# Kernel optimization log

Measured on AMD Instinct MI355X. Metric: run time of the kernel, lower is better.

Reference implementation:

```python
import jax, jax.numpy as jnp
import numpy as np

B, S, D, H = 2, 2048, 1024, 16
DK = D // H

def setup_inputs() -> dict:
    key = jax.random.key(0)
    ks = jax.random.split(key, 12)
    s = 1.0 / np.sqrt(D)
    return {
        "q": jax.random.normal(ks[0], (B, S, D), jnp.float32),
        "k": jax.random.normal(ks[1], (B, S, D), jnp.float32),
        "v": jax.random.normal(ks[2], (B, S, D), jnp.float32),
        "mask": jnp.ones((1, 1, S, S), jnp.int32),
        "Wq": jax.random.normal(ks[3], (D, D), jnp.float32) * s,
        "bq": jnp.zeros((D,), jnp.float32),
        "Wk": jax.random.normal(ks[4], (D, D), jnp.float32) * s,
        "bk": jnp.zeros((D,), jnp.float32),
        "Wv": jax.random.normal(ks[5], (D, D), jnp.float32) * s,
        "bv": jnp.zeros((D,), jnp.float32),
        "Wo": jax.random.normal(ks[6], (D, D), jnp.float32) * s,
        "bo": jnp.zeros((D,), jnp.float32),
    }

def reference(q, k, v, mask, Wq, bq, Wk, bk, Wv, bv, Wo, bo):
    # projections (torch Linear: x @ W^T + b)
    Q = q @ Wq.T + bq
    K = k @ Wk.T + bk
    V = v @ Wv.T + bv
    # split heads: [B,S,D] -> [B,H,S,DK]
    def split(x):
        return x.reshape(B, S, H, DK).transpose(0, 2, 1, 3)
    Qh, Kh, Vh = split(Q), split(K), split(V)
    scores = jnp.einsum('bhqd,bhkd->bhqk', Qh, Kh) / jnp.sqrt(jnp.float32(DK))
    scores = jnp.where(mask == 0, jnp.float32(-1e9), scores)
    attn = jax.nn.softmax(scores, axis=-1)  # dropout p=0.0 -> identity
    x = jnp.einsum('bhqk,bhkd->bhqd', attn, Vh)
    x = x.transpose(0, 2, 1, 3).reshape(B, S, D)
    return x @ Wo.T + bo
```

## Files before the change

kernel.cpp:

```cpp
#include <hip/hip_runtime.h>
#include <hip/hip_bf16.h>
#include <stdint.h>

#define B_    2
#define S_    2048
#define D_    1024
#define H_    16
#define NTOK  (B_ * S_)

typedef __attribute__((ext_vector_type(8))) short bf16x8;
typedef __attribute__((ext_vector_type(4))) float f32x4;
typedef __attribute__((ext_vector_type(2))) float float2v;
typedef __attribute__((ext_vector_type(2))) __bf16 bfv2;

static __device__ __forceinline__ unsigned int pkbf(float a, float b) {
    float2v fv = {a, b};
    bfv2 r = __builtin_convertvector(fv, bfv2);
    unsigned int u;
    __builtin_memcpy(&u, &r, 4);
    return u;
}

using g_cu32 = __attribute__((address_space(1))) const unsigned int;
using l_u32  = __attribute__((address_space(3))) unsigned int;
static __device__ __forceinline__ void gld16(const void* g, void* l) {
    __builtin_amdgcn_global_load_lds((g_cu32*)g, (l_u32*)l, 16, 0, 0);
}

template<int N> static __device__ __forceinline__ void wait_vm() {
    if constexpr (N == 0)      asm volatile("s_waitcnt vmcnt(0)" ::: "memory");
    else if constexpr (N == 2) asm volatile("s_waitcnt vmcnt(2)" ::: "memory");
    else if constexpr (N == 3) asm volatile("s_waitcnt vmcnt(3)" ::: "memory");
    else if constexpr (N == 4) asm volatile("s_waitcnt vmcnt(4)" ::: "memory");
}

#define QN ((size_t)NTOK * D_)
#define WN ((size_t)D_ * D_)

__global__ __launch_bounds__(256) void prep_kernel(
    const float* __restrict__ q, const float* __restrict__ k, const float* __restrict__ v,
    const float* __restrict__ Wq, const float* __restrict__ Wk,
    const float* __restrict__ Wv, const float* __restrict__ Wo,
    const int* __restrict__ mask,
    unsigned short* __restrict__ qb, unsigned short* __restrict__ kb,
    unsigned short* __restrict__ vb, unsigned short* __restrict__ wqb,
    unsigned short* __restrict__ wkb, unsigned short* __restrict__ wvb,
    unsigned short* __restrict__ wob, int* __restrict__ flags) {
    __shared__ int anyz;
    if (blockIdx.x < 8192) {
        size_t i = ((size_t)blockIdx.x * 256 + threadIdx.x) * 8;
        const float* s; unsigned short* d; size_t off;
        if (i < QN)          { s = q; d = qb; off = i; }
        else if (i < 2 * QN) { s = k; d = kb; off = i - QN; }
        else if (i < 3 * QN) { s = v; d = vb; off = i - 2 * QN; }
        else {
            size_t j = i - 3 * QN;
            int wi = (int)(j >> 20);
            s = (wi == 0) ? Wq : (wi == 1) ? Wk : (wi == 2) ? Wv : Wo;
            d = (wi == 0) ? wqb : (wi == 1) ? wkb : (wi == 2) ? wvb : wob;
            off = j & (WN - 1);
        }
        float4 a = *(const float4*)(s + off);
        float4 b = *(const float4*)(s + off + 4);
        uint4 pk;
        pk.x = pkbf(a.x, a.y); pk.y = pkbf(a.z, a.w);
        pk.z = pkbf(b.x, b.y); pk.w = pkbf(b.z, b.w);
        *(uint4*)(d + off) = pk;
    } else {
        if (threadIdx.x == 0) anyz = 0;
        __syncthreads();
        int bid2 = blockIdx.x - 8192;
        const int qt = bid2 >> 5, kt = bid2 & 31;
        int az = 0;
        for (int i = threadIdx.x; i < 64 * 64; i += 256) {
            int r = i >> 6, c = i & 63;
            az |= (mask[(size_t)(qt * 64 + r) * S_ + kt * 64 + c] == 0) ? 1 : 0;
        }
        if (az) atomicOr(&anyz, 1);
        __syncthreads();
        if (threadIdx.x == 0) flags[qt * 32 + kt] = anyz;
    }
}

struct GemmArgs {
    const unsigned short* A[3];
    const unsigned short* W[3];
    const float* bias[3];
    void* C[3];
    int mode[3];
    float scale[3];
};

__global__ __launch_bounds__(512, 2) void gemm_bigM(GemmArgs ga) {
    constexpr int NK = D_ / 32;
    constexpr int AG = 16;
    constexpr int NG = 24;

    const int bid = blockIdx.x;
    const int l = (bid & 7) * 48 + (bid >> 3);
    const int z = l >> 7;
    const int r = l & 127;
    const int bx = r & 15;
    const int by = r >> 4;

    const unsigned short* __restrict__ A = ga.A[z];
    const unsigned short* __restrict__ W = ga.W[z];
    const float* __restrict__ bias = ga.bias[z];
    void* C = ga.C[z];
    const int mode = ga.mode[z];
    const float scl = ga.scale[z];

    __shared__ unsigned short Ls[3][NG * 512];

    const int t    = threadIdx.x;
    const int lane = t & 63;
    const int w    = t >> 6;
    const int fr   = lane & 15;
    const int kq   = lane >> 4;
    const int wrow = w >> 1;
    const int wcol = w & 1;
    const int m0 = bx * 256, n0 = by * 128;

    const int sc = lane >> 4;
    const int sr = lane & 15;

    const unsigned short* gA0 = A + (size_t)(m0 + (2 * w) * 16 + sr) * D_ + sc * 8;
    const unsigned short* gA1 = gA0 + 16 * D_;
    const unsigned short* gB0 = W + (size_t)(n0 + w * 16 + sr) * D_ + sc * 8;
    const int lA0 = (2 * w) * 512, lA1 = (2 * w + 1) * 512, lB0 = (AG + w) * 512;

    int aOff[4], bOff[4];
#pragma unroll
    for (int mi = 0; mi < 4; ++mi) aOff[mi] = (wrow * 4 + mi) * 512 + (kq * 16 + fr) * 8;
#pragma unroll
    for (int ni = 0; ni < 4; ++ni) bOff[ni] = (AG + wcol * 4 + ni) * 512 + (kq * 16 + fr) * 8;

    f32x4 acc[4][4];
#pragma unroll
    for (int i = 0; i < 4; ++i)
#pragma unroll
        for (int j = 0; j < 4; ++j) acc[i][j] = (f32x4)0.0f;

    auto stage = [&](int buf) {
        gld16(gA0, &Ls[buf][lA0]);
        gld16(gA1, &Ls[buf][lA1]);
        gld16(gB0, &Ls[buf][lB0]);
        gA0 += 32; gA1 += 32; gB0 += 32;
    };

    const bool swp = (mode != 2);

    stage(0);
    stage(1);
    int cur = 0;
    for (int k0 = 0; k0 < NK; ++k0) {
        __builtin_amdgcn_sched_barrier(0);
        if (k0 < NK - 1) wait_vm<3>();
        else             wait_vm<0>();
        __builtin_amdgcn_s_barrier();
        __builtin_amdgcn_sched_barrier(0);
        if (k0 + 2 < NK) {
            int pf = (cur >= 1) ? cur - 1 : cur + 2;
            stage(pf);
        }

        bf16x8 af[4], bfr[4];
#pragma unroll
        for (int mi = 0; mi < 4; ++mi) af[mi] = *(const bf16x8*)&Ls[cur][aOff[mi]];
#pragma unroll
        for (int ni = 0; ni < 4; ++ni) bfr[ni] = *(const bf16x8*)&Ls[cur][bOff[ni]];
        if (swp) {
#pragma unroll
            for (int mi = 0; mi < 4; ++mi)
#pragma unroll
                for (int ni = 0; ni < 4; ++ni)
                    acc[mi][ni] = __builtin_amdgcn_mfma_f32_16x16x32_bf16(
                        bfr[ni], af[mi], acc[mi][ni], 0, 0, 0);
        } else {
#pragma unroll
            for (int mi = 0; mi < 4; ++mi)
#pragma unroll
                for (int ni = 0; ni < 4; ++ni)
                    acc[mi][ni] = __builtin_amdgcn_mfma_f32_16x16x32_bf16(
                        af[mi], bfr[ni], acc[mi][ni], 0, 0, 0);
        }
        cur = (cur < 2) ? cur + 1 : 0;
    }

    if (mode == 2) {
        unsigned short* Co = (unsigned short*)C;
#pragma unroll
        for (int ni = 0; ni < 4; ++ni) {
            int col = n0 + wcol * 64 + ni * 16 + fr;
            float bv = bias[col];
            int hh = col >> 6, d = col & 63;
#pragma unroll
            for (int mi = 0; mi < 4; ++mi) {
                int tok = m0 + wrow * 64 + mi * 16 + kq * 4;
                int bb = tok >> 11, sbase = tok & (S_ - 1);
                uint2 pk;
                pk.x = pkbf((acc[mi][ni][0] + bv) * scl, (acc[mi][ni][1] + bv) * scl);
                pk.y = pkbf((acc[mi][ni][2] + bv) * scl, (acc[mi][ni][3] + bv) * scl);
                *(uint2*)(Co + ((size_t)((bb * H_ + hh) * 64 + d)) * S_ + sbase) = pk;
            }
        }
    } else {
        unsigned short* Co = (unsigned short*)C;
#pragma unroll
        for (int ni = 0; ni < 4; ++ni) {
            int nb = n0 + wcol * 64 + ni * 16 + kq * 4;
            float4 b4 = *(const float4*)&bias[nb];
#pragma unroll
            for (int mi = 0; mi < 4; ++mi) {
                int m = m0 + wrow * 64 + mi * 16 + fr;
                uint2 pk;
                pk.x = pkbf((acc[mi][ni][0] + b4.x) * scl, (acc[mi][ni][1] + b4.y) * scl);
                pk.y = pkbf((acc[mi][ni][2] + b4.z) * scl, (acc[mi][ni][3] + b4.w) * scl);
                *(uint2*)(Co + (size_t)m * D_ + nb) = pk;
            }
        }
    }
}

__global__ __launch_bounds__(256, 3) void gemm_out(GemmArgs ga) {
    constexpr int NK = D_ / 32;
    const int bid = blockIdx.x;
    const int l = (bid & 7) * 32 + (bid >> 3);
    const int bx = l & 31;
    const int by = l >> 5;

    const unsigned short* __restrict__ A = ga.A[0];
    const unsigned short* __restrict__ W = ga.W[0];
    const float* __restrict__ bias = ga.bias[0];
    float* Co = (float*)ga.C[0];

    __shared__ unsigned short As[3][8 * 512];
    __shared__ unsigned short Bs[3][8 * 512];

    const int t    = threadIdx.x;
    const int lane = t & 63;
    const int w    = t >> 6;
    const int fr   = lane & 15;
    const int kq   = lane >> 4;
    const int wrow = w >> 1, wcol = w & 1;
    const int m0 = bx * 128, n0 = by * 128;

    const int sc = lane >> 4;
    const int sr = lane & 15;

    const unsigned short* ga0 = A + (size_t)(m0 + (2 * w) * 16 + sr) * D_ + sc * 8;
    const unsigned short* ga1 = ga0 + 16 * D_;
    const unsigned short* gw0 = W + (size_t)(n0 + (2 * w) * 16 + sr) * D_ + sc * 8;
    const unsigned short* gw1 = gw0 + 16 * D_;
    const int la0 = (2 * w) * 512, la1 = (2 * w + 1) * 512;
    const int lw0 = (2 * w) * 512, lw1 = (2 * w + 1) * 512;

    int aOff[4], bOff[4];
#pragma unroll
    for (int mi = 0; mi < 4; ++mi) aOff[mi] = (wrow * 4 + mi) * 512 + (kq * 16 + fr) * 8;
#pragma unroll
    for (int ni = 0; ni < 4; ++ni) bOff[ni] = (wcol * 4 + ni) * 512 + (kq * 16 + fr) * 8;

    f32x4 acc[4][4];
#pragma unroll
    for (int i = 0; i < 4; ++i)
#pragma unroll
        for (int j = 0; j < 4; ++j) acc[i][j] = (f32x4)0.0f;

    auto stage = [&](int buf) {
        gld16(ga0, &As[buf][la0]);
        gld16(ga1, &As[buf][la1]);
        gld16(gw0, &Bs[buf][lw0]);
        gld16(gw1, &Bs[buf][lw1]);
        ga0 += 32; ga1 += 32; gw0 += 32; gw1 += 32;
    };

    stage(0);
    stage(1);
    int cur = 0;
    for (int k0 = 0; k0 < NK; ++k0) {
        __builtin_amdgcn_sched_barrier(0);
        if (k0 < NK - 1) wait_vm<4>();
        else             wait_vm<0>();
        __builtin_amdgcn_s_barrier();
        __builtin_amdgcn_sched_barrier(0);
        if (k0 + 2 < NK) {
            int pf = (cur >= 1) ? cur - 1 : cur + 2;
            stage(pf);
        }

        bf16x8 af[4], bfr[4];
#pragma unroll
        for (int mi = 0; mi < 4; ++mi) af[mi] = *(const bf16x8*)&As[cur][aOff[mi]];
#pragma unroll
        for (int ni = 0; ni < 4; ++ni) bfr[ni] = *(const bf16x8*)&Bs[cur][bOff[ni]];
#pragma unroll
        for (int mi = 0; mi < 4; ++mi)
#pragma unroll
            for (int ni = 0; ni < 4; ++ni)
                acc[mi][ni] = __builtin_amdgcn_mfma_f32_16x16x32_bf16(
                    bfr[ni], af[mi], acc[mi][ni], 0, 0, 0);
        cur = (cur < 2) ? cur + 1 : 0;
    }

#pragma unroll
    for (int ni = 0; ni < 4; ++ni) {
        int nb = n0 + wcol * 64 + ni * 16 + kq * 4;
        float4 b4 = *(const float4*)&bias[nb];
#pragma unroll
        for (int mi = 0; mi < 4; ++mi) {
            int m = m0 + wrow * 64 + mi * 16 + fr;
            float4 o4;
            o4.x = acc[mi][ni][0] + b4.x;
            o4.y = acc[mi][ni][1] + b4.y;
            o4.z = acc[mi][ni][2] + b4.z;
            o4.w = acc[mi][ni][3] + b4.w;
            *(float4*)(Co + (size_t)m * D_ + nb) = o4;
        }
    }
}

__global__ __launch_bounds__(512, 2) void flash4(
    const unsigned short* __restrict__ Qb, const unsigned short* __restrict__ Kb,
    const unsigned short* __restrict__ Vtg, const int* __restrict__ mask,
    const int* __restrict__ flags, unsigned short* __restrict__ Xb) {
    __shared__ unsigned short Ks[3][4096];
    __shared__ unsigned short Vs[3][4096];
    __shared__ unsigned short Ps[16384];

    const int t    = threadIdx.x;
    const int lane = t & 63;
    const int w    = t >> 6;
    const int fr   = lane & 15;
    const int kq   = lane >> 4;
    const int bid = blockIdx.x;
    const int swb = ((bid & 7) << 5) | (bid >> 3);
    const int qt = swb & 7, hd = (swb >> 3) & 15, b = swb >> 7;
    const int q0 = qt * 256;
    const int swz = fr & 7;

    bf16x8 qf[2][2];
#pragma unroll
    for (int qc = 0; qc < 2; ++qc) {
        const unsigned short* qrow_p =
            Qb + (size_t)(b * S_ + q0 + w * 32 + qc * 16 + fr) * D_ + hd * 64;
        qf[qc][0] = *(const bf16x8*)(qrow_p + kq * 8);
        qf[qc][1] = *(const bf16x8*)(qrow_p + 32 + kq * 8);
    }

    unsigned int fmask[2];
#pragma unroll
    for (int qc = 0; qc < 2; ++qc) {
        int qt64 = qt * 4 + ((2 * w + qc) >> 2);
        int fl = (lane < 32) ? flags[qt64 * 32 + lane] : 0;
        fmask[qc] = (unsigned int)__ballot(fl != 0);
    }

    const unsigned short* kptr =
        Kb + (size_t)(b * S_ + (w >> 1) * 16 + fr) * D_ + hd * 64 + (w & 1) * 32 + kq * 8;
    const unsigned short* vptr =
        Vtg + ((size_t)((b * H_ + hd) * 64 + (w >> 1) * 16 + fr)) * S_ + (w & 1) * 32 + kq * 8;

    gld16(kptr, (char*)&Ks[0][0] + w * 1024);
    gld16(vptr, (char*)&Vs[0][0] + w * 1024);
    gld16(kptr + (size_t)64 * D_, (char*)&Ks[1][0] + w * 1024);
    gld16(vptr + 64,              (char*)&Vs[1][0] + w * 1024);
    const unsigned short* kpf = kptr + (size_t)128 * D_;
    const unsigned short* vpf = vptr + 128;

    unsigned short* pswr[2][4];
    const unsigned short* psrd[2][2];
#pragma unroll
    for (int qc = 0; qc < 2; ++qc) {
        int row = w * 32 + qc * 16 + fr;
#pragma unroll
        for (int mi = 0; mi < 4; ++mi) {
            int chunk = mi * 2 + (kq >> 1);
            pswr[qc][mi] = &Ps[row * 64 + ((chunk ^ swz) << 3) + ((kq & 1) << 2)];
        }
#pragma unroll
        for (int kk = 0; kk < 2; ++kk) {
            int c = kk * 4 + kq;
            psrd[qc][kk] = &Ps[row * 64 + ((c ^ swz) << 3)];
        }
    }

    const f32x4 zf = (f32x4)0.0f;
    f32x4 o[2][4];
#pragma unroll
    for (int qc = 0; qc < 2; ++qc)
#pragma unroll
        for (int i = 0; i < 4; ++i) o[qc][i] = zf;
    float2v l2[2];
    l2[0] = (float2v){0.0f, 0.0f};
    l2[1] = (float2v){0.0f, 0.0f};

    auto attn_step = [&](int cur, int kt) {
        f32x4 st[2][4];
#pragma unroll
        for (int mi = 0; mi < 4; ++mi) {
            bf16x8 a = *(const bf16x8*)&Ks[cur][mi * 1024 + (kq * 16 + fr) * 8];
            st[0][mi] = __builtin_amdgcn_mfma_f32_16x16x32_bf16(a, qf[0][0], zf, 0, 0, 0);
            st[1][mi] = __builtin_amdgcn_mfma_f32_16x16x32_bf16(a, qf[1][0], zf, 0, 0, 0);
        }
#pragma unroll
        for (int mi = 0; mi < 4; ++mi) {
            bf16x8 a = *(const bf16x8*)&Ks[cur][mi * 1024 + ((4 + kq) * 16 + fr) * 8];
            st[0][mi] = __builtin_amdgcn_mfma_f32_16x16x32_bf16(a, qf[0][1], st[0][mi], 0, 0, 0);
            st[1][mi] = __builtin_amdgcn_mfma_f32_16x16x32_bf16(a, qf[1][1], st[1][mi], 0, 0, 0);
        }

#pragma unroll
        for (int qc = 0; qc < 2; ++qc) {
            if ((fmask[qc] >> kt) & 1u) {
#pragma unroll
                for (int mi = 0; mi < 4; ++mi) {
                    int4 mv = *(const int4*)&mask[(size_t)(q0 + w * 32 + qc * 16 + fr) * S_ +
                                                  kt * 64 + mi * 16 + kq * 4];
                    if (mv.x == 0) st[qc][mi][0] = -3e8f;
                    if (mv.y == 0) st[qc][mi][1] = -3e8f;
                    if (mv.z == 0) st[qc][mi][2] = -3e8f;
                    if (mv.w == 0) st[qc][mi][3] = -3e8f;
                }
            }
        }

#pragma unroll
        for (int qc = 0; qc < 2; ++qc)
#pragma unroll
            for (int mi = 0; mi < 4; ++mi) {
                float e0 = __builtin_amdgcn_exp2f(st[qc][mi][0]);
                float e1 = __builtin_amdgcn_exp2f(st[qc][mi][1]);
                float e2 = __builtin_amdgcn_exp2f(st[qc][mi][2]);
                float e3 = __builtin_amdgcn_exp2f(st[qc][mi][3]);
                l2[qc] += (float2v){e0, e1} + (float2v){e2, e3};
                uint2 pk;
                pk.x = pkbf(e0, e1);
                pk.y = pkbf(e2, e3);
                *(uint2*)pswr[qc][mi] = pk;
            }

#pragma unroll
        for (int kk = 0; kk < 2; ++kk) {
            bf16x8 pb0 = *(const bf16x8*)psrd[0][kk];
            bf16x8 pb1 = *(const bf16x8*)psrd[1][kk];
#pragma unroll
            for (int mi = 0; mi < 4; ++mi) {
                bf16x8 a = *(const bf16x8*)&Vs[cur][mi * 1024 + ((kk * 4 + kq) * 16 + fr) * 8];
                o[0][mi] = __builtin_amdgcn_mfma_f32_16x16x32_bf16(a, pb0, o[0][mi], 0, 0, 0);
                o[1][mi] = __builtin_amdgcn_mfma_f32_16x16x32_bf16(a, pb1, o[1][mi], 0, 0, 0);
            }
        }
    };

    int cur = 0;
    for (int kt = 0; kt < 31; ++kt) {
        __builtin_amdgcn_sched_barrier(0);
        wait_vm<2>();
        __builtin_amdgcn_s_barrier();
        __builtin_amdgcn_sched_barrier(0);
        if (kt < 30) {
            int pf = (cur >= 1) ? cur - 1 : cur + 2;
            gld16(kpf, (char*)&Ks[pf][0] + w * 1024);
            gld16(vpf, (char*)&Vs[pf][0] + w * 1024);
            kpf += (size_t)64 * D_;
            vpf += 64;
        }
        attn_step(cur, kt);
        cur = (cur < 2) ? cur + 1 : 0;
    }
    __builtin_amdgcn_sched_barrier(0);
    wait_vm<0>();
    __builtin_amdgcn_s_barrier();
    __builtin_amdgcn_sched_barrier(0);
    attn_step(cur, 31);

#pragma unroll
    for (int qc = 0; qc < 2; ++qc) {
        float l_i = l2[qc].x + l2[qc].y;
        l_i += __shfl_xor(l_i, 16, 64);
        l_i += __shfl_xor(l_i, 32, 64);
        float rl = 1.0f / l_i;
#pragma unroll
        for (int mi = 0; mi < 4; ++mi) {
            uint2 pk;
            pk.x = pkbf(o[qc][mi][0] * rl, o[qc][mi][1] * rl);
            pk.y = pkbf(o[qc][mi][2] * rl, o[qc][mi][3] * rl);
            *(uint2*)(Xb + (size_t)(b * S_ + q0 + w * 32 + qc * 16 + fr) * D_ +
                      hd * 64 + mi * 16 + kq * 4) = pk;
        }
    }
}

extern "C" void kernel_launch(void* const* d_in, const int* in_sizes, int n_in,
                              void* d_out, int out_size, void* d_ws, size_t ws_size,
                              hipStream_t stream) {
    const float* q    = (const float*)d_in[0];
    const float* k    = (const float*)d_in[1];
    const float* v    = (const float*)d_in[2];
    const int*   mask = (const int*)d_in[3];
    const float* Wq   = (const float*)d_in[4];
    const float* bq   = (const float*)d_in[5];
    const float* Wk   = (const float*)d_in[6];
    const float* bk   = (const float*)d_in[7];
    const float* Wv   = (const float*)d_in[8];
    const float* bv   = (const float*)d_in[9];
    const float* Wo   = (const float*)d_in[10];
    const float* bo   = (const float*)d_in[11];
    float* out = (float*)d_out;

    unsigned short* qb  = (unsigned short*)d_ws;
    unsigned short* kb  = qb + QN;
    unsigned short* vb  = kb + QN;
    unsigned short* Qf  = vb + QN;
    unsigned short* Kf  = Qf + QN;
    unsigned short* Vt  = Kf + QN;
    unsigned short* wqb = Vt + QN;
    unsigned short* wkb = wqb + WN;
    unsigned short* wvb = wkb + WN;
    unsigned short* wob = wvb + WN;
    int* flags = (int*)(wob + WN);

    const float SC = 0.18033688011112042f;

    prep_kernel<<<9216, 256, 0, stream>>>(q, k, v, Wq, Wk, Wv, Wo, mask,
                                          qb, kb, vb, wqb, wkb, wvb, wob, flags);

    GemmArgs g1;
    g1.A[0] = qb;  g1.W[0] = wqb; g1.bias[0] = bq; g1.C[0] = Qf; g1.mode[0] = 1; g1.scale[0] = SC;
    g1.A[1] = kb;  g1.W[1] = wkb; g1.bias[1] = bk; g1.C[1] = Kf; g1.mode[1] = 1; g1.scale[1] = 1.0f;
    g1.A[2] = vb;  g1.W[2] = wvb; g1.bias[2] = bv; g1.C[2] = Vt; g1.mode[2] = 2; g1.scale[2] = 1.0f;
    gemm_bigM<<<384, 512, 0, stream>>>(g1);

    flash4<<<256, 512, 0, stream>>>(Qf, Kf, Vt, mask, flags, Qf);

    GemmArgs g2;
    g2.A[0] = Qf; g2.W[0] = wob; g2.bias[0] = bo; g2.C[0] = out; g2.mode[0] = 0; g2.scale[0] = 1.0f;
    g2.A[1] = g2.A[2] = nullptr; g2.W[1] = g2.W[2] = nullptr;
    g2.bias[1] = g2.bias[2] = nullptr; g2.C[1] = g2.C[2] = nullptr;
    g2.mode[1] = g2.mode[2] = 0; g2.scale[1] = g2.scale[2] = 1.0f;
    gemm_out<<<256, 256, 0, stream>>>(g2);
}
```

Baseline: 272.8 us.

## Enlarge QKV GEMM tile to 256x256 with BK=64 double buffering

```diff
diff --git a/kernel.cpp b/kernel.cpp
--- a/kernel.cpp
+++ b/kernel.cpp
@@ -30,8 +30,11 @@
 template<int N> static __device__ __forceinline__ void wait_vm() {
     if constexpr (N == 0)      asm volatile("s_waitcnt vmcnt(0)" ::: "memory");
     else if constexpr (N == 2) asm volatile("s_waitcnt vmcnt(2)" ::: "memory");
-    else if constexpr (N == 3) asm volatile("s_waitcnt vmcnt(3)" ::: "memory");
     else if constexpr (N == 4) asm volatile("s_waitcnt vmcnt(4)" ::: "memory");
+    else if constexpr (N == 8) asm volatile("s_waitcnt vmcnt(8)" ::: "memory");
+}
+static __device__ __forceinline__ void wait_lgkm0() {
+    asm volatile("s_waitcnt lgkmcnt(0)" ::: "memory");
 }
 
 #define QN ((size_t)NTOK * D_)
@@ -91,17 +94,15 @@
     float scale[3];
 };
 
-__global__ __launch_bounds__(512, 2) void gemm_bigM(GemmArgs ga) {
-    constexpr int NK = D_ / 32;
-    constexpr int AG = 16;
-    constexpr int NG = 24;
+__global__ __launch_bounds__(512, 2) void gemm_qkv(GemmArgs ga) {
+    constexpr int NK = D_ / 64;
 
     const int bid = blockIdx.x;
-    const int l = (bid & 7) * 48 + (bid >> 3);
-    const int z = l >> 7;
-    const int r = l & 127;
-    const int bx = r & 15;
-    const int by = r >> 4;
+    const int l = (bid & 7) * 24 + (bid >> 3);
+    const int z = l >> 6;
+    const int r = l & 63;
+    const int bx = r >> 2;
+    const int by = r & 3;
 
     const unsigned short* __restrict__ A = ga.A[z];
     const unsigned short* __restrict__ W = ga.W[z];
@@ -110,81 +111,118 @@
     const int mode = ga.mode[z];
     const float scl = ga.scale[z];
 
-    __shared__ unsigned short Ls[3][NG * 512];
+    __shared__ unsigned short As[2][16384];
+    __shared__ unsigned short Bs[2][16384];
 
     const int t    = threadIdx.x;
     const int lane = t & 63;
     const int w    = t >> 6;
     const int fr   = lane & 15;
     const int kq   = lane >> 4;
-    const int wrow = w >> 1;
-    const int wcol = w & 1;
-    const int m0 = bx * 256, n0 = by * 128;
+    const int wrow = w >> 2;
+    const int wcol = w & 3;
+    const int m0 = bx * 256, n0 = by * 256;
 
     const int sc = lane >> 4;
     const int sr = lane & 15;
 
-    const unsigned short* gA0 = A + (size_t)(m0 + (2 * w) * 16 + sr) * D_ + sc * 8;
-    const unsigned short* gA1 = gA0 + 16 * D_;
-    const unsigned short* gB0 = W + (size_t)(n0 + w * 16 + sr) * D_ + sc * 8;
-    const int lA0 = (2 * w) * 512, lA1 = (2 * w + 1) * 512, lB0 = (AG + w) * 512;
-
-    int aOff[4], bOff[4];
-#pragma unroll
-    for (int mi = 0; mi < 4; ++mi) aOff[mi] = (wrow * 4 + mi) * 512 + (kq * 16 + fr) * 8;
-#pragma unroll
-    for (int ni = 0; ni < 4; ++ni) bOff[ni] = (AG + wcol * 4 + ni) * 512 + (kq * 16 + fr) * 8;
-
-    f32x4 acc[4][4];
-#pragma unroll
-    for (int i = 0; i < 4; ++i)
+    const unsigned short* gA[4];
+    const unsigned short* gB[4];
+    int loA[4], loB[4];
+#pragma unroll
+    for (int j = 0; j < 4; ++j) {
+        int g = w * 4 + j;
+        int kh = g >> 4, rb = g & 15;
+        gA[j] = A + (size_t)(m0 + rb * 16 + sr) * D_ + kh * 32 + sc * 8;
+        gB[j] = W + (size_t)(n0 + rb * 16 + sr) * D_ + kh * 32 + sc * 8;
+        loA[j] = g * 512;
+        loB[j] = g * 512;
+    }
+
+    int aOff[2][8], bOff[2][4];
+#pragma unroll
+    for (int kk = 0; kk < 2; ++kk) {
+#pragma unroll
+        for (int mi = 0; mi < 8; ++mi)
+            aOff[kk][mi] = (kk * 16 + wrow * 8 + mi) * 512 + (kq * 16 + fr) * 8;
+#pragma unroll
+        for (int ni = 0; ni < 4; ++ni)
+            bOff[kk][ni] = (kk * 16 + wcol * 4 + ni) * 512 + (kq * 16 + fr) * 8;
+    }
+
+    f32x4 acc[8][4];
+#pragma unroll
+    for (int i = 0; i < 8; ++i)
 #pragma unroll
         for (int j = 0; j < 4; ++j) acc[i][j] = (f32x4)0.0f;
 
     auto stage = [&](int buf) {
-        gld16(gA0, &Ls[buf][lA0]);
-        gld16(gA1, &Ls[buf][lA1]);
-        gld16(gB0, &Ls[buf][lB0]);
-        gA0 += 32; gA1 += 32; gB0 += 32;
+#pragma unroll
+        for (int j = 0; j < 4; ++j) {
+            gld16(gA[j], &As[buf][loA[j]]);
+            gld16(gB[j], &Bs[buf][loB[j]]);
+            gA[j] += 64; gB[j] += 64;
+        }
     };
 
     const bool swp = (mode != 2);
 
     stage(0);
     stage(1);
-    int cur = 0;
     for (int k0 = 0; k0 < NK; ++k0) {
-        __builtin_amdgcn_sched_barrier(0);
-        if (k0 < NK - 1) wait_vm<3>();
+        const int cur = k0 & 1;
+        __builtin_amdgcn_sched_barrier(0);
+        if (k0 < NK - 1) wait_vm<8>();
         else             wait_vm<0>();
         __builtin_amdgcn_s_barrier();
         __builtin_amdgcn_sched_barrier(0);
-        if (k0 + 2 < NK) {
-            int pf = (cur >= 1) ? cur - 1 : cur + 2;
-            stage(pf);
-        }
-
-        bf16x8 af[4], bfr[4];
-#pragma unroll
-        for (int mi = 0; mi < 4; ++mi) af[mi] = *(const bf16x8*)&Ls[cur][aOff[mi]];
-#pragma unroll
-        for (int ni = 0; ni < 4; ++ni) bfr[ni] = *(const bf16x8*)&Ls[cur][bOff[ni]];
-        if (swp) {
-#pragma unroll
-            for (int mi = 0; mi < 4; ++mi)
+
+        {
+            bf16x8 bfr[4];
+#pragma unroll
+            for (int ni = 0; ni < 4; ++ni) bfr[ni] = *(const bf16x8*)&Bs[cur][bOff[0][ni]];
+#pragma unroll
+            for (int mi = 0; mi < 8; ++mi) {
+                bf16x8 a = *(const bf16x8*)&As[cur][aOff[0][mi]];
+                if (swp) {
+#pragma unroll
+                    for (int ni = 0; ni < 4; ++ni)
+                        acc[mi][ni] = __builtin_amdgcn_mfma_f32_16x16x32_bf16(
+                            bfr[ni], a, acc[mi][ni], 0, 0, 0);
+                } else {
+#pragma unroll
+                    for (int ni = 0; ni < 4; ++ni)
+                        acc[mi][ni] = __builtin_amdgcn_mfma_f32_16x16x32_bf16(
+                            a, bfr[ni], acc[mi][ni], 0, 0, 0);
+                }
+            }
+        }
+
+        bf16x8 af1[8], bf1[4];
+#pragma unroll
+        for (int ni = 0; ni < 4; ++ni) bf1[ni] = *(const bf16x8*)&Bs[cur][bOff[1][ni]];
+#pragma unroll
+        for (int mi = 0; mi < 8; ++mi) af1[mi] = *(const bf16x8*)&As[cur][aOff[1][mi]];
+
+        wait_lgkm0();
+        __builtin_amdgcn_sched_barrier(0);
+        __builtin_amdgcn_s_barrier();
+        if (k0 + 2 < NK) stage(cur);
+
+#pragma unroll
+        for (int mi = 0; mi < 8; ++mi) {
+            if (swp) {
 #pragma unroll
                 for (int ni = 0; ni < 4; ++ni)
                     acc[mi][ni] = __builtin_amdgcn_mfma_f32_16x16x32_bf16(
-                        bfr[ni], af[mi], acc[mi][ni], 0, 0, 0);
-        } else {
-#pragma unroll
-            for (int mi = 0; mi < 4; ++mi)
+                        bf1[ni], af1[mi], acc[mi][ni], 0, 0, 0);
+            } else {
 #pragma unroll
                 for (int ni = 0; ni < 4; ++ni)
                     acc[mi][ni] = __builtin_amdgcn_mfma_f32_16x16x32_bf16(
-                        af[mi], bfr[ni], acc[mi][ni], 0, 0, 0);
-        }
-        cur = (cur < 2) ? cur + 1 : 0;
+                        af1[mi], bf1[ni], acc[mi][ni], 0, 0, 0);
+            }
+        }
     }
 
     if (mode == 2) {
@@ -195,8 +233,8 @@
             float bv = bias[col];
             int hh = col >> 6, d = col & 63;
 #pragma unroll
-            for (int mi = 0; mi < 4; ++mi) {
-                int tok = m0 + wrow * 64 + mi * 16 + kq * 4;
+            for (int mi = 0; mi < 8; ++mi) {
+                int tok = m0 + wrow * 128 + mi * 16 + kq * 4;
                 int bb = tok >> 11, sbase = tok & (S_ - 1);
                 uint2 pk;
                 pk.x = pkbf((acc[mi][ni][0] + bv) * scl, (acc[mi][ni][1] + bv) * scl);
@@ -211,8 +249,8 @@
             int nb = n0 + wcol * 64 + ni * 16 + kq * 4;
             float4 b4 = *(const float4*)&bias[nb];
 #pragma unroll
-            for (int mi = 0; mi < 4; ++mi) {
-                int m = m0 + wrow * 64 + mi * 16 + fr;
+            for (int mi = 0; mi < 8; ++mi) {
+                int m = m0 + wrow * 128 + mi * 16 + fr;
                 uint2 pk;
                 pk.x = pkbf((acc[mi][ni][0] + b4.x) * scl, (acc[mi][ni][1] + b4.y) * scl);
                 pk.y = pkbf((acc[mi][ni][2] + b4.z) * scl, (acc[mi][ni][3] + b4.w) * scl);
@@ -530,7 +568,7 @@
     g1.A[0] = qb;  g1.W[0] = wqb; g1.bias[0] = bq; g1.C[0] = Qf; g1.mode[0] = 1; g1.scale[0] = SC;
     g1.A[1] = kb;  g1.W[1] = wkb; g1.bias[1] = bk; g1.C[1] = Kf; g1.mode[1] = 1; g1.scale[1] = 1.0f;
     g1.A[2] = vb;  g1.W[2] = wvb; g1.bias[2] = bv; g1.C[2] = Vt; g1.mode[2] = 2; g1.scale[2] = 1.0f;
-    gemm_bigM<<<384, 512, 0, stream>>>(g1);
+    gemm_qkv<<<192, 512, 0, stream>>>(g1);
 
     flash4<<<256, 512, 0, stream>>>(Qf, Kf, Vt, mask, flags, Qf);
 
```

Measured after the change: 310.9 us. +14.0%, slower.

## Shrink projection GEMM and flash attention tiles to 256-thread blocks

Applied to the files above, without the earlier changes.

```diff
diff --git a/kernel.cpp b/kernel.cpp
--- a/kernel.cpp
+++ b/kernel.cpp
@@ -29,13 +29,14 @@
 
 template<int N> static __device__ __forceinline__ void wait_vm() {
     if constexpr (N == 0)      asm volatile("s_waitcnt vmcnt(0)" ::: "memory");
-    else if constexpr (N == 2) asm volatile("s_waitcnt vmcnt(2)" ::: "memory");
-    else if constexpr (N == 3) asm volatile("s_waitcnt vmcnt(3)" ::: "memory");
     else if constexpr (N == 4) asm volatile("s_waitcnt vmcnt(4)" ::: "memory");
 }
 
 #define QN ((size_t)NTOK * D_)
 #define WN ((size_t)D_ * D_)
+
+struct SwapT { static constexpr bool value = true; };
+struct NoSwapT { static constexpr bool value = false; };
 
 __global__ __launch_bounds__(256) void prep_kernel(
     const float* __restrict__ q, const float* __restrict__ k, const float* __restrict__ v,
@@ -91,18 +92,9 @@
     float scale[3];
 };
 
-__global__ __launch_bounds__(512, 2) void gemm_bigM(GemmArgs ga) {
+__global__ __launch_bounds__(256, 3) void gemm_async(GemmArgs ga) {
     constexpr int NK = D_ / 32;
-    constexpr int AG = 16;
-    constexpr int NG = 24;
-
-    const int bid = blockIdx.x;
-    const int l = (bid & 7) * 48 + (bid >> 3);
-    const int z = l >> 7;
-    const int r = l & 127;
-    const int bx = r & 15;
-    const int by = r >> 4;
-
+    const int z = blockIdx.z;
     const unsigned short* __restrict__ A = ga.A[z];
     const unsigned short* __restrict__ W = ga.W[z];
     const float* __restrict__ bias = ga.bias[z];
@@ -110,30 +102,32 @@
     const int mode = ga.mode[z];
     const float scl = ga.scale[z];
 
-    __shared__ unsigned short Ls[3][NG * 512];
+    __shared__ unsigned short As[3][8 * 512];
+    __shared__ unsigned short Bs[3][8 * 512];
 
     const int t    = threadIdx.x;
     const int lane = t & 63;
     const int w    = t >> 6;
     const int fr   = lane & 15;
     const int kq   = lane >> 4;
-    const int wrow = w >> 1;
-    const int wcol = w & 1;
-    const int m0 = bx * 256, n0 = by * 128;
+    const int wrow = w >> 1, wcol = w & 1;
+    const int m0 = blockIdx.x * 128, n0 = blockIdx.y * 128;
 
     const int sc = lane >> 4;
     const int sr = lane & 15;
 
-    const unsigned short* gA0 = A + (size_t)(m0 + (2 * w) * 16 + sr) * D_ + sc * 8;
-    const unsigned short* gA1 = gA0 + 16 * D_;
-    const unsigned short* gB0 = W + (size_t)(n0 + w * 16 + sr) * D_ + sc * 8;
-    const int lA0 = (2 * w) * 512, lA1 = (2 * w + 1) * 512, lB0 = (AG + w) * 512;
+    const unsigned short* ga0 = A + (size_t)(m0 + (2 * w) * 16 + sr) * D_ + sc * 8;
+    const unsigned short* ga1 = ga0 + 16 * D_;
+    const unsigned short* gw0 = W + (size_t)(n0 + (2 * w) * 16 + sr) * D_ + sc * 8;
+    const unsigned short* gw1 = gw0 + 16 * D_;
+    const int la0 = (2 * w) * 512, la1 = (2 * w + 1) * 512;
+    const int lw0 = (2 * w) * 512, lw1 = (2 * w + 1) * 512;
 
     int aOff[4], bOff[4];
 #pragma unroll
     for (int mi = 0; mi < 4; ++mi) aOff[mi] = (wrow * 4 + mi) * 512 + (kq * 16 + fr) * 8;
 #pragma unroll
-    for (int ni = 0; ni < 4; ++ni) bOff[ni] = (AG + wcol * 4 + ni) * 512 + (kq * 16 + fr) * 8;
+    for (int ni = 0; ni < 4; ++ni) bOff[ni] = (wcol * 4 + ni) * 512 + (kq * 16 + fr) * 8;
 
     f32x4 acc[4][4];
 #pragma unroll
@@ -142,50 +136,56 @@
         for (int j = 0; j < 4; ++j) acc[i][j] = (f32x4)0.0f;
 
     auto stage = [&](int buf) {
-        gld16(gA0, &Ls[buf][lA0]);
-        gld16(gA1, &Ls[buf][lA1]);
-        gld16(gB0, &Ls[buf][lB0]);
-        gA0 += 32; gA1 += 32; gB0 += 32;
+        gld16(ga0, &As[buf][la0]);
+        gld16(ga1, &As[buf][la1]);
+        gld16(gw0, &Bs[buf][lw0]);
+        gld16(gw1, &Bs[buf][lw1]);
+        ga0 += 32; ga1 += 32; gw0 += 32; gw1 += 32;
     };
 
-    const bool swp = (mode != 2);
-
-    stage(0);
-    stage(1);
-    int cur = 0;
-    for (int k0 = 0; k0 < NK; ++k0) {
+    auto kloop = [&](auto swc) {
+        constexpr bool SW = decltype(swc)::value;
+        auto mma_step = [&](int cur) {
+            bf16x8 af[4], bfr[4];
+#pragma unroll
+            for (int mi = 0; mi < 4; ++mi) af[mi] = *(const bf16x8*)&As[cur][aOff[mi]];
+#pragma unroll
+            for (int ni = 0; ni < 4; ++ni) bfr[ni] = *(const bf16x8*)&Bs[cur][bOff[ni]];
+#pragma unroll
+            for (int mi = 0; mi < 4; ++mi)
+#pragma unroll
+                for (int ni = 0; ni < 4; ++ni) {
+                    if constexpr (SW)
+                        acc[mi][ni] = __builtin_amdgcn_mfma_f32_16x16x32_bf16(
+                            bfr[ni], af[mi], acc[mi][ni], 0, 0, 0);
+                    else
+                        acc[mi][ni] = __builtin_amdgcn_mfma_f32_16x16x32_bf16(
+                            af[mi], bfr[ni], acc[mi][ni], 0, 0, 0);
+                }
+        };
+
+        stage(0);
+        stage(1);
+        int cur = 0;
+        for (int k0 = 0; k0 < NK - 1; ++k0) {
+            __builtin_amdgcn_sched_barrier(0);
+            wait_vm<4>();
+            __builtin_amdgcn_s_barrier();
+            __builtin_amdgcn_sched_barrier(0);
+            if (k0 + 2 < NK) {
+                int pf = (cur >= 1) ? cur - 1 : cur + 2;
+                stage(pf);
+            }
+            mma_step(cur);
+            cur = (cur < 2) ? cur + 1 : 0;
+        }
         __builtin_amdgcn_sched_barrier(0);
-        if (k0 < NK - 1) wait_vm<3>();
-        else             wait_vm<0>();
+        wait_vm<0>();
         __builtin_amdgcn_s_barrier();
         __builtin_amdgcn_sched_barrier(0);
-        if (k0 + 2 < NK) {
-            int pf = (cur >= 1) ? cur - 1 : cur + 2;
-            stage(pf);
-        }
-
-        bf16x8 af[4], bfr[4];
-#pragma unroll
-        for (int mi = 0; mi < 4; ++mi) af[mi] = *(const bf16x8*)&Ls[cur][aOff[mi]];
-#pragma unroll
-        for (int ni = 0; ni < 4; ++ni) bfr[ni] = *(const bf16x8*)&Ls[cur][bOff[ni]];
-        if (swp) {
-#pragma unroll
-            for (int mi = 0; mi < 4; ++mi)
-#pragma unroll
-                for (int ni = 0; ni < 4; ++ni)
-                    acc[mi][ni] = __builtin_amdgcn_mfma_f32_16x16x32_bf16(
-                        bfr[ni], af[mi], acc[mi][ni], 0, 0, 0);
-        } else {
-#pragma unroll
-            for (int mi = 0; mi < 4; ++mi)
-#pragma unroll
-                for (int ni = 0; ni < 4; ++ni)
-                    acc[mi][ni] = __builtin_amdgcn_mfma_f32_16x16x32_bf16(
-                        af[mi], bfr[ni], acc[mi][ni], 0, 0, 0);
-        }
-        cur = (cur < 2) ? cur + 1 : 0;
-    }
+        mma_step(cur);
+    };
+    if (mode == 2) kloop(NoSwapT{}); else kloop(SwapT{});
 
     if (mode == 2) {
         unsigned short* Co = (unsigned short*)C;
@@ -320,13 +320,13 @@
     }
 }
 
-__global__ __launch_bounds__(512, 2) void flash4(
+__global__ __launch_bounds__(256, 2) void flash4(
     const unsigned short* __restrict__ Qb, const unsigned short* __restrict__ Kb,
     const unsigned short* __restrict__ Vtg, const int* __restrict__ mask,
     const int* __restrict__ flags, unsigned short* __restrict__ Xb) {
     __shared__ unsigned short Ks[3][4096];
     __shared__ unsigned short Vs[3][4096];
-    __shared__ unsigned short Ps[16384];
+    __shared__ unsigned short Ps[8192];
 
     const int t    = threadIdx.x;
     const int lane = t & 63;
@@ -334,9 +334,9 @@
     const int fr   = lane & 15;
     const int kq   = lane >> 4;
     const int bid = blockIdx.x;
-    const int swb = ((bid & 7) << 5) | (bid >> 3);
-    const int qt = swb & 7, hd = (swb >> 3) & 15, b = swb >> 7;
-    const int q0 = qt * 256;
+    const int swb = ((bid & 7) << 6) | (bid >> 3);
+    const int qt = swb & 15, hd = (swb >> 4) & 15, b = swb >> 8;
+    const int q0 = qt * 128;
     const int swz = fr & 7;
 
     bf16x8 qf[2][2];
@@ -351,22 +351,27 @@
     unsigned int fmask[2];
 #pragma unroll
     for (int qc = 0; qc < 2; ++qc) {
-        int qt64 = qt * 4 + ((2 * w + qc) >> 2);
+        int qt64 = qt * 2 + ((2 * w + qc) >> 1);
         int fl = (lane < 32) ? flags[qt64 * 32 + lane] : 0;
         fmask[qc] = (unsigned int)__ballot(fl != 0);
     }
 
-    const unsigned short* kptr =
-        Kb + (size_t)(b * S_ + (w >> 1) * 16 + fr) * D_ + hd * 64 + (w & 1) * 32 + kq * 8;
-    const unsigned short* vptr =
-        Vtg + ((size_t)((b * H_ + hd) * 64 + (w >> 1) * 16 + fr)) * S_ + (w & 1) * 32 + kq * 8;
-
-    gld16(kptr, (char*)&Ks[0][0] + w * 1024);
-    gld16(vptr, (char*)&Vs[0][0] + w * 1024);
-    gld16(kptr + (size_t)64 * D_, (char*)&Ks[1][0] + w * 1024);
-    gld16(vptr + 64,              (char*)&Vs[1][0] + w * 1024);
-    const unsigned short* kpf = kptr + (size_t)128 * D_;
-    const unsigned short* vpf = vptr + 128;
+    const unsigned short* kp0 =
+        Kb + (size_t)(b * S_ + w * 16 + fr) * D_ + hd * 64 + kq * 8;
+    const unsigned short* vp0 =
+        Vtg + ((size_t)((b * H_ + hd) * 64 + w * 16 + fr)) * S_ + kq * 8;
+
+    auto stageKV = [&](int buf, const unsigned short* kp, const unsigned short* vp) {
+        gld16(kp,      (char*)&Ks[buf][0] + w * 2048);
+        gld16(kp + 32, (char*)&Ks[buf][0] + w * 2048 + 1024);
+        gld16(vp,      (char*)&Vs[buf][0] + w * 2048);
+        gld16(vp + 32, (char*)&Vs[buf][0] + w * 2048 + 1024);
+    };
+
+    stageKV(0, kp0, vp0);
+    stageKV(1, kp0 + (size_t)64 * D_, vp0 + 64);
+    const unsigned short* kpf = kp0 + (size_t)128 * D_;
+    const unsigned short* vpf = vp0 + 128;
 
     unsigned short* pswr[2][4];
     const unsigned short* psrd[2][2];
@@ -456,13 +461,12 @@
     int cur = 0;
     for (int kt = 0; kt < 31; ++kt) {
         __builtin_amdgcn_sched_barrier(0);
-        wait_vm<2>();
+        wait_vm<4>();
         __builtin_amdgcn_s_barrier();
         __builtin_amdgcn_sched_barrier(0);
         if (kt < 30) {
             int pf = (cur >= 1) ? cur - 1 : cur + 2;
-            gld16(kpf, (char*)&Ks[pf][0] + w * 1024);
-            gld16(vpf, (char*)&Vs[pf][0] + w * 1024);
+            stageKV(pf, kpf, vpf);
             kpf += (size_t)64 * D_;
             vpf += 64;
         }
@@ -530,9 +534,9 @@
     g1.A[0] = qb;  g1.W[0] = wqb; g1.bias[0] = bq; g1.C[0] = Qf; g1.mode[0] = 1; g1.scale[0] = SC;
     g1.A[1] = kb;  g1.W[1] = wkb; g1.bias[1] = bk; g1.C[1] = Kf; g1.mode[1] = 1; g1.scale[1] = 1.0f;
     g1.A[2] = vb;  g1.W[2] = wvb; g1.bias[2] = bv; g1.C[2] = Vt; g1.mode[2] = 2; g1.scale[2] = 1.0f;
-    gemm_bigM<<<384, 512, 0, stream>>>(g1);
-
-    flash4<<<256, 512, 0, stream>>>(Qf, Kf, Vt, mask, flags, Qf);
+    gemm_async<<<dim3(NTOK / 128, D_ / 128, 3), 256, 0, stream>>>(g1);
+
+    flash4<<<512, 256, 0, stream>>>(Qf, Kf, Vt, mask, flags, Qf);
 
     GemmArgs g2;
     g2.A[0] = Qf; g2.W[0] = wob; g2.bias[0] = bo; g2.C[0] = out; g2.mode[0] = 0; g2.scale[0] = 1.0f;
```

After: 299.3 us. 9.7% more time.
